# Kernel tuning notes

Hardware: AMD Instinct MI355X
Metric: run time of the kernel (lower is better)

## Reference

```python
import jax, jax.numpy as jnp
import numpy as np

B, T, E, H = 4, 1024, 512, 8
DH = E // H  # head dim = 64


def setup_inputs() -> dict:
    key = jax.random.key(0)
    ks = jax.random.split(key, 6)
    s = 1.0 / np.sqrt(E)
    return {
        "q": jax.random.normal(ks[0], (B, T, E), dtype=jnp.float32),
        "kv": jax.random.normal(ks[1], (B, T, E), dtype=jnp.float32),
        "Wq": jax.random.normal(ks[2], (E, E), dtype=jnp.float32) * s,
        "Wk": jax.random.normal(ks[3], (E, E), dtype=jnp.float32) * s,
        "Wv": jax.random.normal(ks[4], (E, E), dtype=jnp.float32) * s,
        "Wo": jax.random.normal(ks[5], (E, E), dtype=jnp.float32) * s,
        "head_num": H,
    }


def _split_heads_dh(x, h):
    # einops 'b t (d h)' with h=head_num: head index is FASTEST in channel dim
    b, t, e = x.shape
    d = e // h
    return x.reshape(b, t, d, h).transpose(0, 3, 1, 2)  # (b, h, t, d)


def reference(q, kv, Wq, Wk, Wv, Wo, head_num):
    e = q.shape[-1]
    dk = (e // head_num) ** 0.5  # NOTE: multiplied, per original code

    qp = q @ Wq   # weights stored as (in, out); Linear(bias=False)
    kp = kv @ Wk
    vp = kv @ Wv

    query = _split_heads_dh(qp, head_num)  # (b, h, t, d)
    key = _split_heads_dh(kp, head_num)
    value = _split_heads_dh(vp, head_num)

    qf = jnp.fft.fftn(query, axes=(-2, -1))  # complex, over (t, d)
    kf = jnp.fft.fftn(key, axes=(-2, -1))

    # complex einsum, key NOT conjugated (faithful to torch source)
    energy = jnp.einsum("bhid,bhjd->bhij", qf, kf) * dk
    energy = jnp.fft.ifftn(energy, axes=(-2, -1)).real  # (b, h, t, t)

    attention = jax.nn.softmax(energy, axis=-1)
    out = jnp.einsum("bhij,bhjd->bhid", attention, value)  # (b, h, t, d)

    # einops 'b h t d -> b t (h d)': head index SLOWEST in output channel dim
    b, h, t, d = out.shape
    out = out.transpose(0, 2, 1, 3).reshape(b, t, h * d)
    return out @ Wo
```

## Files before the change

kernel.cpp:

```cpp
#include <hip/hip_runtime.h>
#include <math.h>

#define BB 4
#define TT 1024
#define EE 512
#define HH 8
#define DD 64
#define BT (BB * TT)

typedef _Float16 f16;
typedef __attribute__((ext_vector_type(8))) _Float16 f16x8;
typedef __attribute__((ext_vector_type(4))) float f32x4;

__global__ __launch_bounds__(256) void prep_k(
    const float* __restrict__ q, const float* __restrict__ kv,
    const float* __restrict__ Wq, const float* __restrict__ Wk,
    const float* __restrict__ Wv, const float* __restrict__ Wo,
    f16* __restrict__ wqh, f16* __restrict__ wql,
    f16* __restrict__ wkh, f16* __restrict__ wkl,
    f16* __restrict__ wvh, f16* __restrict__ woh,
    f16* __restrict__ qAhi, f16* __restrict__ qAlo,
    f16* __restrict__ kvAhi, f16* __restrict__ kvAlo) {
    const int t = threadIdx.x;
    const int y = blockIdx.y;
    if (y < 4) {
        int idx = blockIdx.x * 256 + t;
        int k = idx & (EE - 1);
        int n = idx >> 9;
        if (y == 0) {
            float v = Wq[k * EE + n] * 512.0f;
            f16 hi = (f16)v;
            wqh[n * EE + k] = hi;
            wql[n * EE + k] = (f16)(v - (float)hi);
        } else if (y == 1) {
            int d = n >> 3, h = n & 7;
            int sn = (((DD - d) & (DD - 1)) << 3) | h;
            float v = Wk[k * EE + sn];
            f16 hi = (f16)v;
            wkh[n * EE + k] = hi;
            wkl[n * EE + k] = (f16)(v - (float)hi);
        } else if (y == 2) {
            wvh[n * EE + k] = (f16)Wv[k * EE + n];
        } else {
            woh[n * EE + k] = (f16)Wo[k * EE + n];
        }
    } else {
        const float* src = (y == 4) ? q : kv;
        f16* dh = (y == 4) ? qAhi : kvAhi;
        f16* dl = (y == 4) ? qAlo : kvAlo;
        int base = (blockIdx.x * 256 + t) * 8;
        float4 a = *(const float4*)&src[base];
        float4 c = *(const float4*)&src[base + 4];
        float xs[8] = {a.x, a.y, a.z, a.w, c.x, c.y, c.z, c.w};
        f16x8 hi, lo;
#pragma unroll
        for (int e = 0; e < 8; ++e) {
            f16 hh = (f16)xs[e];
            hi[e] = hh;
            lo[e] = (f16)(xs[e] - (float)hh);
        }
        *(f16x8*)&dh[base] = hi;
        *(f16x8*)&dl[base] = lo;
    }
}

__global__ __launch_bounds__(256) void proj_k(
    const f16* __restrict__ qAhi, const f16* __restrict__ qAlo,
    const f16* __restrict__ kvAhi, const f16* __restrict__ kvAlo,
    const f16* __restrict__ wqh, const f16* __restrict__ wql,
    const f16* __restrict__ wkh, const f16* __restrict__ wkl,
    const f16* __restrict__ wvh,
    f16* __restrict__ qhi, f16* __restrict__ qlo,
    f16* __restrict__ khi, f16* __restrict__ klo, f16* __restrict__ vP) {
    __shared__ __align__(16) f16 Ah_s[2][128][40];
    __shared__ __align__(16) f16 Al_s[2][128][40];
    __shared__ __align__(16) f16 Wh_s[2][64][40];
    __shared__ __align__(16) f16 Wl_s[2][64][40];
    __shared__ __align__(16) f16 Wv_s[2][64][40];
    f16 (*Ep)[136] = reinterpret_cast<f16(*)[136]>(&Ah_s[0][0][0]);

    const int t = threadIdx.x;
    const int w = t >> 6, l = t & 63;
    const int wm = w >> 1, wn = w & 1;
    const int fr = l & 15, fc = l >> 4;
    const int m0b = blockIdx.x * 128;
    const int n0b = blockIdx.y * 64;
    const int z   = blockIdx.z;
    const int ar = t >> 1, ak = t & 1;
    const int wr = t >> 2, wc = t & 3;

    const f16* AH = z ? kvAhi : qAhi;
    const f16* AL = z ? kvAlo : qAlo;
    const f16* WH = z ? wkh : wqh;
    const f16* WL = z ? wkl : wql;

    f32x4 accK[4][2], accV[4][2];
#pragma unroll
    for (int i = 0; i < 4; ++i)
#pragma unroll
        for (int j = 0; j < 2; ++j) {
            accK[i][j] = f32x4{0.f, 0.f, 0.f, 0.f};
            accV[i][j] = f32x4{0.f, 0.f, 0.f, 0.f};
        }

    f16x8 ahA[2], alA[2], whA, wlA, wvA;
    f16x8 ahB[2], alB[2], whB, wlB, wvB;

    auto loadSet = [&](int k0, f16x8 (&ah)[2], f16x8 (&al)[2],
                       f16x8& wh, f16x8& wl, f16x8& wv) {
        size_t aoff = (size_t)(m0b + ar) * EE + k0 + ak * 16;
        ah[0] = *(const f16x8*)&AH[aoff];
        ah[1] = *(const f16x8*)&AH[aoff + 8];
        al[0] = *(const f16x8*)&AL[aoff];
        al[1] = *(const f16x8*)&AL[aoff + 8];
        size_t woff = (size_t)(n0b + wr) * EE + k0 + wc * 8;
        wh = *(const f16x8*)&WH[woff];
        wl = *(const f16x8*)&WL[woff];
        if (z) wv = *(const f16x8*)&wvh[woff];
    };
    auto stageSet = [&](int bf, f16x8 (&ah)[2], f16x8 (&al)[2],
                        f16x8& wh, f16x8& wl, f16x8& wv) {
        *(f16x8*)&Ah_s[bf][ar][ak * 16]     = ah[0];
        *(f16x8*)&Ah_s[bf][ar][ak * 16 + 8] = ah[1];
        *(f16x8*)&Al_s[bf][ar][ak * 16]     = al[0];
        *(f16x8*)&Al_s[bf][ar][ak * 16 + 8] = al[1];
        *(f16x8*)&Wh_s[bf][wr][wc * 8] = wh;
        *(f16x8*)&Wl_s[bf][wr][wc * 8] = wl;
        if (z) *(f16x8*)&Wv_s[bf][wr][wc * 8] = wv;
    };
    auto comp = [&](int bf) {
        f16x8 Ahf[4], Alf[4], Bh[2], Bl[2], Bv[2];
#pragma unroll
        for (int mi = 0; mi < 4; ++mi) {
            Ahf[mi] = *(const f16x8*)&Ah_s[bf][wm * 64 + mi * 16 + fr][fc * 8];
            Alf[mi] = *(const f16x8*)&Al_s[bf][wm * 64 + mi * 16 + fr][fc * 8];
        }
#pragma unroll
        for (int nj = 0; nj < 2; ++nj) {
            Bh[nj] = *(const f16x8*)&Wh_s[bf][wn * 32 + nj * 16 + fr][fc * 8];
            Bl[nj] = *(const f16x8*)&Wl_s[bf][wn * 32 + nj * 16 + fr][fc * 8];
            if (z) Bv[nj] = *(const f16x8*)&Wv_s[bf][wn * 32 + nj * 16 + fr][fc * 8];
        }
        __builtin_amdgcn_s_setprio(1);
#pragma unroll
        for (int mi = 0; mi < 4; ++mi)
#pragma unroll
            for (int nj = 0; nj < 2; ++nj) {
                accK[mi][nj] = __builtin_amdgcn_mfma_f32_16x16x32_f16(
                    Ahf[mi], Bh[nj], accK[mi][nj], 0, 0, 0);
                accK[mi][nj] = __builtin_amdgcn_mfma_f32_16x16x32_f16(
                    Ahf[mi], Bl[nj], accK[mi][nj], 0, 0, 0);
                accK[mi][nj] = __builtin_amdgcn_mfma_f32_16x16x32_f16(
                    Alf[mi], Bh[nj], accK[mi][nj], 0, 0, 0);
                if (z)
                    accV[mi][nj] = __builtin_amdgcn_mfma_f32_16x16x32_f16(
                        Ahf[mi], Bv[nj], accV[mi][nj], 0, 0, 0);
            }
        __builtin_amdgcn_s_setprio(0);
    };

    loadSet(0, ahA, alA, whA, wlA, wvA);
    stageSet(0, ahA, alA, whA, wlA, wvA);
    loadSet(32, ahA, alA, whA, wlA, wvA);
    loadSet(64, ahB, alB, whB, wlB, wvB);
    __syncthreads();

    for (int ks = 0; ks < 16; ks += 2) {
        comp(0);
        stageSet(1, ahA, alA, whA, wlA, wvA);
        if (ks + 3 < 16) loadSet((ks + 3) * 32, ahA, alA, whA, wlA, wvA);
        __syncthreads();
        comp(1);
        if (ks + 2 < 16) stageSet(0, ahB, alB, whB, wlB, wvB);
        if (ks + 4 < 16) loadSet((ks + 4) * 32, ahB, alB, whB, wlB, wvB);
        __syncthreads();
    }

    f16* dsthi = z ? khi : qhi;
    f16* dstlo = z ? klo : qlo;
#pragma unroll
    for (int mi = 0; mi < 4; ++mi)
#pragma unroll
        for (int nj = 0; nj < 2; ++nj)
#pragma unroll
            for (int r = 0; r < 4; ++r)
                Ep[wn * 32 + nj * 16 + fr][wm * 64 + mi * 16 + fc * 4 + r] =
                    (f16)accK[mi][nj][r];
    __syncthreads();
#pragma unroll
    for (int i = 0; i < 4; ++i) {
        int task = t * 4 + i;
        int mr = task >> 3, h = task & 7;
        f16x8 v;
#pragma unroll
        for (int d = 0; d < 8; ++d) v[d] = Ep[8 * d + h][mr];
        *(f16x8*)&dsthi[((size_t)h * BT + m0b + mr) * DD + (n0b >> 3)] = v;
    }
    __syncthreads();
#pragma unroll
    for (int mi = 0; mi < 4; ++mi)
#pragma unroll
        for (int nj = 0; nj < 2; ++nj)
#pragma unroll
            for (int r = 0; r < 4; ++r) {
                float x = accK[mi][nj][r];
                f16 hh = (f16)x;
                Ep[wn * 32 + nj * 16 + fr][wm * 64 + mi * 16 + fc * 4 + r] =
                    (f16)(x - (float)hh);
            }
    __syncthreads();
#pragma unroll
    for (int i = 0; i < 4; ++i) {
        int task = t * 4 + i;
        int mr = task >> 3, h = task & 7;
        f16x8 v;
#pragma unroll
        for (int d = 0; d < 8; ++d) v[d] = Ep[8 * d + h][mr];
        *(f16x8*)&dstlo[((size_t)h * BT + m0b + mr) * DD + (n0b >> 3)] = v;
    }
    if (z) {
        __syncthreads();
#pragma unroll
        for (int mi = 0; mi < 4; ++mi)
#pragma unroll
            for (int nj = 0; nj < 2; ++nj)
#pragma unroll
                for (int r = 0; r < 4; ++r)
                    Ep[wn * 32 + nj * 16 + fr][wm * 64 + mi * 16 + fc * 4 + r] =
                        (f16)accV[mi][nj][r];
        __syncthreads();
#pragma unroll
        for (int i = 0; i < 4; ++i) {
            int task = t * 4 + i;
            int mg = task & 15, nn = task >> 4;
            int h = nn & 7, dl = nn >> 3;
            int d = (n0b >> 3) + dl;
            int koff = m0b + mg * 8;
            int tile = koff >> 6;
            int kf   = (koff >> 5) & 1;
            int lg2  = (koff >> 3) & 3;
            int dvt  = d >> 4, lqd = d & 15;
            f16x8 v = *(const f16x8*)&Ep[nn][mg * 8];
            size_t off = (((((size_t)h * 64 + tile) * 2 + kf) * 4 + dvt) * 64 +
                          lg2 * 16 + lqd) * 8;
            *(f16x8*)&vP[off] = v;
        }
    }
}

__global__ __launch_bounds__(256) void outmm_k(const f16* __restrict__ Af,
                                               const f16* __restrict__ WThi,
                                               float* __restrict__ out) {
    __shared__ __align__(16) f16 Ah_s[2][64][72];
    __shared__ __align__(16) f16 Wh_s[2][64][72];

    const int t = threadIdx.x;
    const int w = t >> 6, l = t & 63;
    const int wm = w >> 1, wn = w & 1;
    const int fr = l & 15, fc = l >> 4;
    const int m0b = blockIdx.x * 64;
    const int n0b = blockIdx.y * 64;
    const int sr = t >> 2, sch = t & 3;

    f32x4 acc[2][2];
#pragma unroll
    for (int i = 0; i < 2; ++i)
#pragma unroll
        for (int j = 0; j < 2; ++j) acc[i][j] = f32x4{0.f, 0.f, 0.f, 0.f};

    f16x8 af[2], wf[2];
    auto loadAB = [&](int k0) {
#pragma unroll
        for (int i = 0; i < 2; ++i) {
            af[i] = *(const f16x8*)&Af[(size_t)(m0b + sr) * EE + k0 + sch * 16 + i * 8];
            wf[i] = *(const f16x8*)&WThi[(size_t)(n0b + sr) * EE + k0 + sch * 16 + i * 8];
        }
    };
    auto stage = [&](int bf) {
#pragma unroll
        for (int i = 0; i < 2; ++i) {
            *(f16x8*)&Ah_s[bf][sr][sch * 16 + i * 8] = af[i];
            *(f16x8*)&Wh_s[bf][sr][sch * 16 + i * 8] = wf[i];
        }
    };

    loadAB(0);
    stage(0);
    __syncthreads();
    int cur = 0;
    for (int ks = 0; ks < 8; ++ks) {
        if (ks < 7) loadAB((ks + 1) * 64);
        f16x8 Ahf[2][2], Bhf[2][2];
#pragma unroll
        for (int mi = 0; mi < 2; ++mi)
#pragma unroll
            for (int kb = 0; kb < 2; ++kb)
                Ahf[mi][kb] =
                    *(const f16x8*)&Ah_s[cur][wm * 32 + mi * 16 + fr][kb * 32 + fc * 8];
#pragma unroll
        for (int nj = 0; nj < 2; ++nj)
#pragma unroll
            for (int kb = 0; kb < 2; ++kb)
                Bhf[nj][kb] =
                    *(const f16x8*)&Wh_s[cur][wn * 32 + nj * 16 + fr][kb * 32 + fc * 8];
        __builtin_amdgcn_s_setprio(1);
#pragma unroll
        for (int mi = 0; mi < 2; ++mi)
#pragma unroll
            for (int nj = 0; nj < 2; ++nj)
#pragma unroll
                for (int kb = 0; kb < 2; ++kb)
                    acc[mi][nj] = __builtin_amdgcn_mfma_f32_16x16x32_f16(
                        Ahf[mi][kb], Bhf[nj][kb], acc[mi][nj], 0, 0, 0);
        __builtin_amdgcn_s_setprio(0);
        if (ks < 7) stage(cur ^ 1);
        __syncthreads();
        cur ^= 1;
    }

#pragma unroll
    for (int mi = 0; mi < 2; ++mi)
#pragma unroll
        for (int nj = 0; nj < 2; ++nj)
#pragma unroll
            for (int r = 0; r < 4; ++r)
                out[(size_t)(m0b + wm * 32 + mi * 16 + fc * 4 + r) * EE +
                    n0b + wn * 32 + nj * 16 + fr] = acc[mi][nj][r];
}

__global__ __launch_bounds__(256) void attn_mfma_k(const f16* __restrict__ qhiP,
    const f16* __restrict__ qloP, const f16* __restrict__ khiP,
    const f16* __restrict__ kloP, const f16* __restrict__ vP,
    f16* __restrict__ ctx) {
    __shared__ __align__(16) f16 Khi[2][64][64];
    __shared__ __align__(16) f16 Klo[2][64][64];
    __shared__ __align__(16) f16 Pl[4][16][88];

    const int bid = blockIdx.x;
    const int swz = (bid & 7) * 64 + (bid >> 3);
    const int bx = swz & 15;
    const int h  = (swz >> 4) & 7;
    const int b  = swz >> 7;

    const int t  = threadIdx.x;
    const int w  = t >> 6;
    const int l  = t & 63;
    const int lg = l >> 4;
    const int lq = l & 15;
    const int q0 = bx * 64 + w * 16;
    const size_t plane = ((size_t)h * BT + (size_t)b * TT) * DD;

    f16x8 Qhi[2], Qlo[2];
#pragma unroll
    for (int kf = 0; kf < 2; ++kf) {
        size_t qo = plane + (size_t)(q0 + lq) * DD + kf * 32 + lg * 8;
        Qhi[kf] = *(const f16x8*)&qhiP[qo];
        Qlo[kf] = *(const f16x8*)&qloP[qo];
    }

    f32x4 Oacc[4];
#pragma unroll
    for (int i = 0; i < 4; ++i) Oacc[i] = f32x4{0.f, 0.f, 0.f, 0.f};
    float m = -1e30f, lsum = 0.f;

    const int sr = t >> 2, sch = t & 3;
    f16x8 kh[2], kl[2];

    auto loadK = [&](int kt0) {
        size_t off = plane + (size_t)(kt0 + sr) * DD + sch * 16;
        kh[0] = *(const f16x8*)&khiP[off];
        kh[1] = *(const f16x8*)&khiP[off + 8];
        kl[0] = *(const f16x8*)&kloP[off];
        kl[1] = *(const f16x8*)&kloP[off + 8];
    };
    auto stageK = [&](int bf) {
#pragma unroll
        for (int i = 0; i < 2; ++i) {
            int chunk = sch * 2 + i;
            int dsw = chunk ^ (sr & 7);
            *(f16x8*)&Khi[bf][sr][dsw * 8] = kh[i];
            *(f16x8*)&Klo[bf][sr][dsw * 8] = kl[i];
        }
    };

    f16x8 bvA[2][4], bvB[2][4];
    auto loadBV = [&](int kt0, f16x8 (&bv)[2][4]) {
        const f16* tb = vP + ((size_t)h * 64 + ((b * TT + kt0) >> 6)) * 4096;
#pragma unroll
        for (int kf = 0; kf < 2; ++kf)
#pragma unroll
            for (int dvt = 0; dvt < 4; ++dvt)
                bv[kf][dvt] = *(const f16x8*)&tb[((kf * 4 + dvt) * 64 + l) * 8];
    };

    f32x4 ScA[4], ScB[4];
    auto QK = [&](int curb, f32x4 (&Sc)[4]) {
        __builtin_amdgcn_s_setprio(1);
#pragma unroll
        for (int kt = 0; kt < 4; ++kt) {
            f32x4 c = f32x4{0.f, 0.f, 0.f, 0.f};
            int keyr = kt * 16 + lq;
#pragma unroll
            for (int kf = 0; kf < 2; ++kf) {
                int sw = (kf * 4 + lg) ^ (keyr & 7);
                f16x8 ahi = *(const f16x8*)&Khi[curb][keyr][sw * 8];
                f16x8 alo = *(const f16x8*)&Klo[curb][keyr][sw * 8];
                c = __builtin_amdgcn_mfma_f32_16x16x32_f16(ahi, Qhi[kf], c, 0, 0, 0);
                c = __builtin_amdgcn_mfma_f32_16x16x32_f16(ahi, Qlo[kf], c, 0, 0, 0);
                c = __builtin_amdgcn_mfma_f32_16x16x32_f16(alo, Qhi[kf], c, 0, 0, 0);
            }
            Sc[kt] = c;
        }
        __builtin_amdgcn_s_setprio(0);
    };

    auto SMPV = [&](const f32x4 (&Sc)[4], const f16x8 (&bv)[2][4]) {
        float sv[16];
#pragma unroll
        for (int kt = 0; kt < 4; ++kt)
#pragma unroll
            for (int r = 0; r < 4; ++r) sv[kt * 4 + r] = Sc[kt][r];
        float tm = sv[0];
#pragma unroll
        for (int i = 1; i < 16; ++i) tm = fmaxf(tm, sv[i]);
        tm = fmaxf(tm, __shfl_xor(tm, 16));
        tm = fmaxf(tm, __shfl_xor(tm, 32));

        bool skip = __all(tm <= m + 8.0f);
        float Mn = m, corr = 1.0f;
        if (!skip) {
            Mn = fmaxf(m, tm);
            corr = __expf(m - Mn);
        }
        float ps = 0.f;
        f16 ph[16];
#pragma unroll
        for (int i = 0; i < 16; ++i) {
            float p = __expf(sv[i] - Mn);
            ps += p;
            ph[i] = (f16)p;
        }
        ps += __shfl_xor(ps, 16);
        ps += __shfl_xor(ps, 32);
        if (skip) {
            lsum += ps;
        } else {
            lsum = lsum * corr + ps;
            m = Mn;
        }

#pragma unroll
        for (int kt = 0; kt < 4; ++kt)
#pragma unroll
            for (int rp = 0; rp < 4; rp += 2) {
                union { f16 h; unsigned short u; } u0, u1;
                u0.h = ph[kt * 4 + rp]; u1.h = ph[kt * 4 + rp + 1];
                unsigned int pk = ((unsigned int)u1.u << 16) | u0.u;
                *(unsigned int*)&Pl[w][lq][kt * 16 + lg * 4 + rp] = pk;
            }

        if (!skip) {
            float cq[4];
#pragma unroll
            for (int r = 0; r < 4; ++r) cq[r] = __shfl(corr, lg * 4 + r);
#pragma unroll
            for (int dvt = 0; dvt < 4; ++dvt)
#pragma unroll
                for (int r = 0; r < 4; ++r) Oacc[dvt][r] *= cq[r];
        }

        __builtin_amdgcn_s_setprio(1);
#pragma unroll
        for (int kf = 0; kf < 2; ++kf) {
            f16x8 pa = *(const f16x8*)&Pl[w][lq][kf * 32 + lg * 8];
#pragma unroll
            for (int dvt = 0; dvt < 4; ++dvt)
                Oacc[dvt] = __builtin_amdgcn_mfma_f32_16x16x32_f16(
                    pa, bv[kf][dvt], Oacc[dvt], 0, 0, 0);
        }
        __builtin_amdgcn_s_setprio(0);
    };

    loadK(0);
    stageK(0);
    loadK(64);
    loadBV(0, bvA);
    __syncthreads();
    QK(0, ScA);
    stageK(1);
    __syncthreads();

    for (int t2 = 0; t2 < 16; t2 += 2) {
        const int kt0 = t2 << 6;
        loadBV(kt0 + 64, bvB);
        if (t2 + 2 < 16) loadK(kt0 + 128);
        QK(1, ScB);
        SMPV(ScA, bvA);
        if (t2 + 2 < 16) stageK(0);
        __syncthreads();
        if (t2 + 2 < 16) loadBV(kt0 + 128, bvA);
        if (t2 + 3 < 16) loadK(kt0 + 192);
        if (t2 + 2 < 16) QK(0, ScA);
        SMPV(ScB, bvB);
        if (t2 + 3 < 16) stageK(1);
        if (t2 + 2 < 16) __syncthreads();
    }

    float linv = 1.0f / lsum;
    float lq4[4];
#pragma unroll
    for (int r = 0; r < 4; ++r) lq4[r] = __shfl(linv, lg * 4 + r);
#pragma unroll
    for (int r = 0; r < 4; ++r) {
        f16* crow = ctx + (size_t)(b * TT + q0 + lg * 4 + r) * EE + h * DD;
#pragma unroll
        for (int dvt = 0; dvt < 4; ++dvt)
            crow[dvt * 16 + lq] = (f16)(Oacc[dvt][r] * lq4[r]);
    }
}

extern "C" void kernel_launch(void* const* d_in, const int* in_sizes, int n_in,
                              void* d_out, int out_size, void* d_ws, size_t ws_size,
                              hipStream_t stream) {
    const float* q  = (const float*)d_in[0];
    const float* kv = (const float*)d_in[1];
    const float* Wq = (const float*)d_in[2];
    const float* Wk = (const float*)d_in[3];
    const float* Wv = (const float*)d_in[4];
    const float* Wo = (const float*)d_in[5];
    float* out = (float*)d_out;

    f16* ws = (f16*)d_ws;
    const size_t PL  = (size_t)HH * BT * DD;
    const size_t WPL = (size_t)EE * EE;
    f16* qhi   = ws + 0 * PL;
    f16* qlo   = ws + 1 * PL;
    f16* khi   = ws + 2 * PL;
    f16* klo   = ws + 3 * PL;
    f16* vPck  = ws + 4 * PL;
    f16* ctx   = ws + 5 * PL;
    f16* qAhi  = ws + 6 * PL;
    f16* qAlo  = ws + 7 * PL;
    f16* kvAhi = ws + 8 * PL;
    f16* kvAlo = ws + 9 * PL;
    f16* wqh = ws + 10 * PL;
    f16* wql = wqh + 1 * WPL;
    f16* wkh = wqh + 2 * WPL;
    f16* wkl = wqh + 3 * WPL;
    f16* wvh = wqh + 4 * WPL;
    f16* woh = wqh + 5 * WPL;

    prep_k<<<dim3(1024, 6), dim3(256), 0, stream>>>(
        q, kv, Wq, Wk, Wv, Wo, wqh, wql, wkh, wkl, wvh, woh,
        qAhi, qAlo, kvAhi, kvAlo);

    proj_k<<<dim3(BT / 128, EE / 64, 2), dim3(256), 0, stream>>>(
        qAhi, qAlo, kvAhi, kvAlo, wqh, wql, wkh, wkl, wvh,
        qhi, qlo, khi, klo, vPck);

    attn_mfma_k<<<dim3(512), dim3(256), 0, stream>>>(
        qhi, qlo, khi, klo, vPck, ctx);

    outmm_k<<<dim3(BT / 64, EE / 64), dim3(256), 0, stream>>>(ctx, woh, out);
}
```

Baseline: 78.00 us.

## Pre-pack K into MFMA fragment layout and load directly to registers

The projection kernel now writes the K hi/lo planes in a layout already matching the MFMA A-operand fragments for each 16-key subtile. The attention kernel then loads K fragments straight from global memory into registers with coalesced per-lane 16-byte loads. This drops the shared-memory staging buffers, the swizzled LDS reads and the block-wide barriers in the main loop. In exchange, every wave of a block fetches the same K data separately from global memory or cache, which multiplies K traffic by the number of waves. The loop also relies on register double-buffering across subtiles to hide global load latency.

Measured after the change: 78.17 us. No clear change (+0.2%).

```diff
diff --git a/kernel.cpp b/kernel.cpp
--- a/kernel.cpp
+++ b/kernel.cpp
@@ -71,7 +71,7 @@
     const f16* __restrict__ wkh, const f16* __restrict__ wkl,
     const f16* __restrict__ wvh,
     f16* __restrict__ qhi, f16* __restrict__ qlo,
-    f16* __restrict__ khi, f16* __restrict__ klo, f16* __restrict__ vP) {
+    f16* __restrict__ kthi, f16* __restrict__ ktlo, f16* __restrict__ vP) {
     __shared__ __align__(16) f16 Ah_s[2][128][40];
     __shared__ __align__(16) f16 Al_s[2][128][40];
     __shared__ __align__(16) f16 Wh_s[2][64][40];
@@ -176,8 +176,9 @@
         __syncthreads();
     }
 
-    f16* dsthi = z ? khi : qhi;
-    f16* dstlo = z ? klo : qlo;
+    const int d0  = n0b >> 3;
+    const int kfc = d0 >> 5;
+    const int lg2 = (d0 >> 3) & 3;
 #pragma unroll
     for (int mi = 0; mi < 4; ++mi)
 #pragma unroll
@@ -194,7 +195,16 @@
         f16x8 v;
 #pragma unroll
         for (int d = 0; d < 8; ++d) v[d] = Ep[8 * d + h][mr];
-        *(f16x8*)&dsthi[((size_t)h * BT + m0b + mr) * DD + (n0b >> 3)] = v;
+        if (z == 0) {
+            *(f16x8*)&qhi[((size_t)h * BT + m0b + mr) * DD + d0] = v;
+        } else {
+            int mg = m0b + mr;
+            int bb = mg >> 10, key = mg & 1023;
+            size_t off = ((((((size_t)h * BB + bb) * 16 + (key >> 6)) * 4 +
+                            ((key >> 4) & 3)) * 2 + kfc) * 64 +
+                          lg2 * 16 + (key & 15)) * 8;
+            *(f16x8*)&kthi[off] = v;
+        }
     }
     __syncthreads();
 #pragma unroll
@@ -216,7 +226,16 @@
         f16x8 v;
 #pragma unroll
         for (int d = 0; d < 8; ++d) v[d] = Ep[8 * d + h][mr];
-        *(f16x8*)&dstlo[((size_t)h * BT + m0b + mr) * DD + (n0b >> 3)] = v;
+        if (z == 0) {
+            *(f16x8*)&qlo[((size_t)h * BT + m0b + mr) * DD + d0] = v;
+        } else {
+            int mg = m0b + mr;
+            int bb = mg >> 10, key = mg & 1023;
+            size_t off = ((((((size_t)h * BB + bb) * 16 + (key >> 6)) * 4 +
+                            ((key >> 4) & 3)) * 2 + kfc) * 64 +
+                          lg2 * 16 + (key & 15)) * 8;
+            *(f16x8*)&ktlo[off] = v;
+        }
     }
     if (z) {
         __syncthreads();
@@ -234,15 +253,15 @@
             int task = t * 4 + i;
             int mg = task & 15, nn = task >> 4;
             int h = nn & 7, dl = nn >> 3;
-            int d = (n0b >> 3) + dl;
+            int d = d0 + dl;
             int koff = m0b + mg * 8;
             int tile = koff >> 6;
             int kf   = (koff >> 5) & 1;
-            int lg2  = (koff >> 3) & 3;
+            int lgv  = (koff >> 3) & 3;
             int dvt  = d >> 4, lqd = d & 15;
             f16x8 v = *(const f16x8*)&Ep[nn][mg * 8];
             size_t off = (((((size_t)h * 64 + tile) * 2 + kf) * 4 + dvt) * 64 +
-                          lg2 * 16 + lqd) * 8;
+                          lgv * 16 + lqd) * 8;
             *(f16x8*)&vP[off] = v;
         }
     }
@@ -329,11 +348,9 @@
 }
 
 __global__ __launch_bounds__(256) void attn_mfma_k(const f16* __restrict__ qhiP,
-    const f16* __restrict__ qloP, const f16* __restrict__ khiP,
-    const f16* __restrict__ kloP, const f16* __restrict__ vP,
+    const f16* __restrict__ qloP, const f16* __restrict__ kthiP,
+    const f16* __restrict__ ktloP, const f16* __restrict__ vP,
     f16* __restrict__ ctx) {
-    __shared__ __align__(16) f16 Khi[2][64][64];
-    __shared__ __align__(16) f16 Klo[2][64][64];
     __shared__ __align__(16) f16 Pl[4][16][88];
 
     const int bid = blockIdx.x;
@@ -363,55 +380,38 @@
     for (int i = 0; i < 4; ++i) Oacc[i] = f32x4{0.f, 0.f, 0.f, 0.f};
     float m = -1e30f, lsum = 0.f;
 
-    const int sr = t >> 2, sch = t & 3;
-    f16x8 kh[2], kl[2];
-
-    auto loadK = [&](int kt0) {
-        size_t off = plane + (size_t)(kt0 + sr) * DD + sch * 16;
-        kh[0] = *(const f16x8*)&khiP[off];
-        kh[1] = *(const f16x8*)&khiP[off + 8];
-        kl[0] = *(const f16x8*)&kloP[off];
-        kl[1] = *(const f16x8*)&kloP[off + 8];
-    };
-    auto stageK = [&](int bf) {
-#pragma unroll
-        for (int i = 0; i < 2; ++i) {
-            int chunk = sch * 2 + i;
-            int dsw = chunk ^ (sr & 7);
-            *(f16x8*)&Khi[bf][sr][dsw * 8] = kh[i];
-            *(f16x8*)&Klo[bf][sr][dsw * 8] = kl[i];
-        }
+    const f16* khb = kthiP + (((size_t)h * BB + b) << 16);
+    const f16* klb = ktloP + (((size_t)h * BB + b) << 16);
+
+    f16x8 kA[4], kB[4];
+    auto LK = [&](int kt64, int kt, f16x8 (&s)[4]) {
+        size_t o = ((size_t)kt64 * 4 + kt) * 1024 + l * 8;
+        s[0] = *(const f16x8*)&khb[o];
+        s[1] = *(const f16x8*)&khb[o + 512];
+        s[2] = *(const f16x8*)&klb[o];
+        s[3] = *(const f16x8*)&klb[o + 512];
+    };
+    auto QK1 = [&](const f16x8 (&s)[4]) -> f32x4 {
+        f32x4 c = f32x4{0.f, 0.f, 0.f, 0.f};
+        __builtin_amdgcn_s_setprio(1);
+        c = __builtin_amdgcn_mfma_f32_16x16x32_f16(s[0], Qhi[0], c, 0, 0, 0);
+        c = __builtin_amdgcn_mfma_f32_16x16x32_f16(s[0], Qlo[0], c, 0, 0, 0);
+        c = __builtin_amdgcn_mfma_f32_16x16x32_f16(s[2], Qhi[0], c, 0, 0, 0);
+        c = __builtin_amdgcn_mfma_f32_16x16x32_f16(s[1], Qhi[1], c, 0, 0, 0);
+        c = __builtin_amdgcn_mfma_f32_16x16x32_f16(s[1], Qlo[1], c, 0, 0, 0);
+        c = __builtin_amdgcn_mfma_f32_16x16x32_f16(s[3], Qhi[1], c, 0, 0, 0);
+        __builtin_amdgcn_s_setprio(0);
+        return c;
     };
 
     f16x8 bvA[2][4], bvB[2][4];
-    auto loadBV = [&](int kt0, f16x8 (&bv)[2][4]) {
-        const f16* tb = vP + ((size_t)h * 64 + ((b * TT + kt0) >> 6)) * 4096;
+    auto loadBV = [&](int tile, f16x8 (&bv)[2][4]) {
+        const f16* tb = vP + ((size_t)h * 64 + b * 16 + tile) * 4096;
 #pragma unroll
         for (int kf = 0; kf < 2; ++kf)
 #pragma unroll
             for (int dvt = 0; dvt < 4; ++dvt)
                 bv[kf][dvt] = *(const f16x8*)&tb[((kf * 4 + dvt) * 64 + l) * 8];
-    };
-
-    f32x4 ScA[4], ScB[4];
-    auto QK = [&](int curb, f32x4 (&Sc)[4]) {
-        __builtin_amdgcn_s_setprio(1);
-#pragma unroll
-        for (int kt = 0; kt < 4; ++kt) {
-            f32x4 c = f32x4{0.f, 0.f, 0.f, 0.f};
-            int keyr = kt * 16 + lq;
-#pragma unroll
-            for (int kf = 0; kf < 2; ++kf) {
-                int sw = (kf * 4 + lg) ^ (keyr & 7);
-                f16x8 ahi = *(const f16x8*)&Khi[curb][keyr][sw * 8];
-                f16x8 alo = *(const f16x8*)&Klo[curb][keyr][sw * 8];
-                c = __builtin_amdgcn_mfma_f32_16x16x32_f16(ahi, Qhi[kf], c, 0, 0, 0);
-                c = __builtin_amdgcn_mfma_f32_16x16x32_f16(ahi, Qlo[kf], c, 0, 0, 0);
-                c = __builtin_amdgcn_mfma_f32_16x16x32_f16(alo, Qhi[kf], c, 0, 0, 0);
-            }
-            Sc[kt] = c;
-        }
-        __builtin_amdgcn_s_setprio(0);
     };
 
     auto SMPV = [&](const f32x4 (&Sc)[4], const f16x8 (&bv)[2][4]) {
@@ -481,29 +481,24 @@
         __builtin_amdgcn_s_setprio(0);
     };
 
-    loadK(0);
-    stageK(0);
-    loadK(64);
+    LK(0, 0, kA);
     loadBV(0, bvA);
-    __syncthreads();
-    QK(0, ScA);
-    stageK(1);
-    __syncthreads();
-
-    for (int t2 = 0; t2 < 16; t2 += 2) {
-        const int kt0 = t2 << 6;
-        loadBV(kt0 + 64, bvB);
-        if (t2 + 2 < 16) loadK(kt0 + 128);
-        QK(1, ScB);
-        SMPV(ScA, bvA);
-        if (t2 + 2 < 16) stageK(0);
-        __syncthreads();
-        if (t2 + 2 < 16) loadBV(kt0 + 128, bvA);
-        if (t2 + 3 < 16) loadK(kt0 + 192);
-        if (t2 + 2 < 16) QK(0, ScA);
-        SMPV(ScB, bvB);
-        if (t2 + 3 < 16) stageK(1);
-        if (t2 + 2 < 16) __syncthreads();
+    f32x4 Sc[4];
+
+    for (int tile = 0; tile < 16; tile += 2) {
+        LK(tile, 1, kB);      Sc[0] = QK1(kA);
+        LK(tile, 2, kA);      Sc[1] = QK1(kB);
+        LK(tile, 3, kB);      Sc[2] = QK1(kA);
+        LK(tile + 1, 0, kA);  Sc[3] = QK1(kB);
+        loadBV(tile + 1, bvB);
+        SMPV(Sc, bvA);
+        LK(tile + 1, 1, kB);  Sc[0] = QK1(kA);
+        LK(tile + 1, 2, kA);  Sc[1] = QK1(kB);
+        LK(tile + 1, 3, kB);  Sc[2] = QK1(kA);
+        if (tile + 2 < 16) LK(tile + 2, 0, kA);
+        Sc[3] = QK1(kB);
+        if (tile + 2 < 16) loadBV(tile + 2, bvA);
+        SMPV(Sc, bvB);
     }
 
     float linv = 1.0f / lsum;
@@ -535,8 +530,8 @@
     const size_t WPL = (size_t)EE * EE;
     f16* qhi   = ws + 0 * PL;
     f16* qlo   = ws + 1 * PL;
-    f16* khi   = ws + 2 * PL;
-    f16* klo   = ws + 3 * PL;
+    f16* kthi  = ws + 2 * PL;
+    f16* ktlo  = ws + 3 * PL;
     f16* vPck  = ws + 4 * PL;
     f16* ctx   = ws + 5 * PL;
     f16* qAhi  = ws + 6 * PL;
@@ -556,10 +551,10 @@
 
     proj_k<<<dim3(BT / 128, EE / 64, 2), dim3(256), 0, stream>>>(
         qAhi, qAlo, kvAhi, kvAlo, wqh, wql, wkh, wkl, wvh,
-        qhi, qlo, khi, klo, vPck);
+        qhi, qlo, kthi, ktlo, vPck);
 
     attn_mfma_k<<<dim3(512), dim3(256), 0, stream>>>(
-        qhi, qlo, khi, klo, vPck, ctx);
+        qhi, qlo, kthi, ktlo, vPck, ctx);
 
     outmm_k<<<dim3(BT / 64, EE / 64), dim3(256), 0, stream>>>(ctx, woh, out);
 }
```
